# Kernel optimization log

Measured on AMD Instinct MI355X. Metric: run time of the kernel, lower is better.

Reference implementation:

```python
import jax, jax.numpy as jnp
import numpy as np

D_MODEL = 1024
N_HEADS = 16
D_LATENT = 64
LN_EPS = 1e-5


def setup_inputs() -> dict:
    key = jax.random.key(0)
    ks = jax.random.split(key, 9)
    dm, h, dl = D_MODEL, N_HEADS, D_LATENT
    hd = h * dl
    # xavier_uniform with gain=0.1: limit = 0.1 * sqrt(6/(fan_in+fan_out))
    def xavier(k, fan_in, fan_out):
        lim = 0.1 * np.sqrt(6.0 / (fan_in + fan_out))
        return jax.random.uniform(k, (fan_in, fan_out), jnp.float32, -lim, lim)
    return {
        "x": jax.random.normal(ks[0], (4, 2048, dm), jnp.float32),
        "ln_g": jnp.ones((dm,), jnp.float32),
        "ln_b": jnp.zeros((dm,), jnp.float32),
        "wq": xavier(ks[1], dm, hd), "bq": jnp.zeros((hd,), jnp.float32),
        "wk": xavier(ks[2], dm, hd), "bk": jnp.zeros((hd,), jnp.float32),
        "wv": xavier(ks[3], dm, hd), "bv": jnp.zeros((hd,), jnp.float32),
        "wo": xavier(ks[4], hd, dm), "bo": jnp.zeros((dm,), jnp.float32),
    }


def reference(x, ln_g, ln_b, wq, bq, wk, bk, wv, bv, wo, bo):
    b, s, dm = x.shape
    h, dl = N_HEADS, D_LATENT
    # context = raw x (bound before LayerNorm in the torch code)
    context = x
    mu = jnp.mean(x, axis=-1, keepdims=True)
    var = jnp.var(x, axis=-1, keepdims=True)
    xn = (x - mu) * jax.lax.rsqrt(var + LN_EPS) * ln_g + ln_b
    q = (xn @ wq + bq).reshape(b, s, h, dl).transpose(0, 2, 1, 3)          # b h s d
    k = (context @ wk + bk).reshape(b, -1, h, dl).transpose(0, 2, 1, 3)    # b h t d
    v = (context @ wv + bv).reshape(b, -1, h, dl).transpose(0, 2, 1, 3)
    scores = jnp.einsum("bhsd,bhtd->bhst", q, k) / jnp.sqrt(jnp.float32(dl))
    attn = jax.nn.softmax(scores.astype(jnp.float32), axis=-1)
    # dropout omitted (eval mode / deterministic reference)
    out = jnp.einsum("bhst,bhtd->bhsd", attn, v)
    out = out.transpose(0, 2, 1, 3).reshape(b, s, h * dl)
    return out @ wo + bo
```

## Files before the change

### kernel.cpp

```cpp
#include <hip/hip_runtime.h>
#include <cstdint>

typedef __attribute__((ext_vector_type(8))) __bf16 bf16x8;
typedef __attribute__((ext_vector_type(8))) unsigned short u16x8;
typedef __attribute__((ext_vector_type(4))) unsigned short u16x4;
typedef __attribute__((ext_vector_type(4))) float f32x4;
typedef __attribute__((ext_vector_type(2))) unsigned int u32x2;
typedef __attribute__((ext_vector_type(4))) unsigned int u32x4;

__device__ inline unsigned short f2bf(float f) {
  return __builtin_bit_cast(unsigned short, (__bf16)f);
}

__device__ inline void llds16(const void* g, void* l) {
  __builtin_amdgcn_global_load_lds((const uint32_t*)g, (uint32_t*)l, 16, 0, 0);
}

__device__ inline bf16x8 ldfrag(const unsigned short* p) {
  u16x8 v = *(const u16x8*)p;
  return __builtin_bit_cast(bf16x8, v);
}

__device__ inline f32x4 mfma16(bf16x8 a, bf16x8 b, f32x4 c) {
  return __builtin_amdgcn_mfma_f32_16x16x32_bf16(a, b, c, 0, 0, 0);
}

__global__ __launch_bounds__(256) void ln_kernel(
    const float* __restrict__ x, const float* __restrict__ g, const float* __restrict__ be,
    unsigned short* __restrict__ xn, unsigned short* __restrict__ xb)
{
  const int row = blockIdx.x, tid = threadIdx.x;
  const size_t base = (size_t)row * 1024 + tid * 4;
  float4 v = *(const float4*)&x[base];
  float s  = v.x + v.y + v.z + v.w;
  float sq = v.x*v.x + v.y*v.y + v.z*v.z + v.w*v.w;
#pragma unroll
  for (int o = 1; o < 64; o <<= 1) { s += __shfl_xor(s, o); sq += __shfl_xor(sq, o); }
  __shared__ float ls[8];
  if ((tid & 63) == 0) { ls[tid >> 6] = s; ls[4 + (tid >> 6)] = sq; }
  __syncthreads();
  s  = ls[0] + ls[1] + ls[2] + ls[3];
  sq = ls[4] + ls[5] + ls[6] + ls[7];
  const float mu   = s * (1.f / 1024.f);
  const float var  = sq * (1.f / 1024.f) - mu * mu;
  const float rstd = rsqrtf(var + 1e-5f);
  float4 gv = *(const float4*)&g[tid * 4];
  float4 bv = *(const float4*)&be[tid * 4];
  u16x4 a, bb;
  a[0] = f2bf((v.x - mu) * rstd * gv.x + bv.x);
  a[1] = f2bf((v.y - mu) * rstd * gv.y + bv.y);
  a[2] = f2bf((v.z - mu) * rstd * gv.z + bv.z);
  a[3] = f2bf((v.w - mu) * rstd * gv.w + bv.w);
  bb[0] = f2bf(v.x); bb[1] = f2bf(v.y); bb[2] = f2bf(v.z); bb[3] = f2bf(v.w);
  *(u16x4*)&xn[base] = a;
  *(u16x4*)&xb[base] = bb;
}

__global__ __launch_bounds__(256) void wcast_kernel(
    const float* __restrict__ wq, const float* __restrict__ wk,
    const float* __restrict__ wv, const float* __restrict__ wo,
    unsigned short* __restrict__ wT, unsigned short* __restrict__ woT)
{
  __shared__ float t[64][66];
  const int z = blockIdx.z;
  const float* W = (z == 0) ? wq : (z == 1) ? wk : (z == 2) ? wv : wo;
  unsigned short* O = (z < 3) ? (wT + (size_t)z * 1048576) : woT;
  const int n0 = blockIdx.x * 64, k0 = blockIdx.y * 64;
  for (int idx = threadIdx.x; idx < 4096; idx += 256) {
    int r = idx >> 6, c = idx & 63;
    t[r][c] = W[(size_t)(k0 + r) * 1024 + n0 + c];
  }
  __syncthreads();
  for (int idx = threadIdx.x; idx < 4096; idx += 256) {
    int r = idx >> 6, c = idx & 63;
    O[(size_t)(n0 + r) * 1024 + k0 + c] = f2bf(t[c][r]);
  }
}

__global__ __launch_bounds__(256) void vtrans_kernel(
    const unsigned short* __restrict__ V, unsigned short* __restrict__ VT)
{
  __shared__ unsigned short t[64][66];
  const int bh = blockIdx.y, t0 = blockIdx.x * 64;
  const unsigned short* src = V + (size_t)bh * 131072 + (size_t)t0 * 64;
  for (int idx = threadIdx.x; idx < 4096; idx += 256) {
    int r = idx >> 6, c = idx & 63;
    t[r][c] = src[(size_t)r * 64 + c];
  }
  __syncthreads();
  unsigned short* dst = VT + (size_t)bh * 131072 + t0;
  for (int idx = threadIdx.x; idx < 4096; idx += 256) {
    int r = idx >> 6, c = idx & 63;
    dst[(size_t)r * 2048 + c] = t[c][r];
  }
}

template<int MODE>
__global__ __launch_bounds__(256) void gemm_kernel(
    const unsigned short* __restrict__ A0, const unsigned short* __restrict__ A1,
    const unsigned short* __restrict__ BT,
    const float* __restrict__ b0, const float* __restrict__ b1, const float* __restrict__ b2,
    void* __restrict__ Cv, int M, int N, int K)
{
  __shared__ unsigned short S[32768];
  const int tid = threadIdx.x;
  const int wave = tid >> 6, lane = tid & 63;
  const int l15 = lane & 15, l4 = lane >> 4;
  const int swz = (l15 & 7) << 3;
  const int NBN = N >> 7;
  const int nwg = gridDim.x, cpx = nwg >> 3;
  const int orig = blockIdx.x;
  const int id = (orig & 7) * cpx + (orig >> 3);
  const int bn = id % NBN, bm = id / NBN;
  const int m0 = bm * 128, n0 = bn * 128;
  const unsigned short* Ap = (MODE == 0 && bn >= 8) ? A1 : A0;
  const int wr = (wave >> 1) * 64, wc = (wave & 1) * 64;

  f32x4 acc[4][4];
#pragma unroll
  for (int m = 0; m < 4; m++)
#pragma unroll
    for (int n = 0; n < 4; n++) acc[m][n] = {0.f, 0.f, 0.f, 0.f};

  auto STAGE = [&](int b, int kt) {
#pragma unroll
    for (int r = 0; r < 4; r++) {
      int D = r * 4096 + tid * 16;
      int row = D >> 7;
      int colus = ((D & 127) >> 1) ^ ((row & 7) << 3);
      llds16(&Ap[(size_t)(m0 + row) * K + kt + colus], &S[b * 16384 + r * 2048 + wave * 512]);
      llds16(&BT[(size_t)(n0 + row) * K + kt + colus],
             &S[b * 16384 + 8192 + r * 2048 + wave * 512]);
    }
  };

  const int KSTEPS = K >> 6;
  int cur = 0;
  STAGE(0, 0);
  for (int ki = 0; ki < KSTEPS; ki++) {
    if (ki < KSTEPS - 1) {
      STAGE(cur ^ 1, (ki + 1) << 6);
      asm volatile("s_waitcnt vmcnt(8)" ::: "memory");
    } else {
      asm volatile("s_waitcnt vmcnt(0)" ::: "memory");
    }
    __builtin_amdgcn_s_barrier();
    __builtin_amdgcn_sched_barrier(0);
    const unsigned short* Asb = &S[cur * 16384];
    const unsigned short* Bsb = &S[cur * 16384 + 8192];
#pragma unroll
    for (int ks = 0; ks < 2; ks++) {
      bf16x8 af[4], bfr[4];
#pragma unroll
      for (int m = 0; m < 4; m++)
        af[m]  = ldfrag(&Asb[(wr + m * 16 + l15) * 64 + ((ks * 32 + l4 * 8) ^ swz)]);
#pragma unroll
      for (int n = 0; n < 4; n++)
        bfr[n] = ldfrag(&Bsb[(wc + n * 16 + l15) * 64 + ((ks * 32 + l4 * 8) ^ swz)]);
#pragma unroll
      for (int m = 0; m < 4; m++)
#pragma unroll
        for (int n = 0; n < 4; n++)
          acc[m][n] = mfma16(af[m], bfr[n], acc[m][n]);
    }
    __builtin_amdgcn_s_barrier();
    cur ^= 1;
  }

#pragma unroll
  for (int nf = 0; nf < 4; nf++) {
    int c = n0 + wc + nf * 16 + l15;
    float bias; float sc = 1.0f;
    if (MODE == 0) {
      int sec = c >> 10;
      bias = (sec == 0 ? b0 : (sec == 1 ? b1 : b2))[c & 1023];
      if (sec == 0) sc = 0.18033688011112042f;
    } else {
      bias = b0[c];
    }
#pragma unroll
    for (int mf = 0; mf < 4; mf++) {
#pragma unroll
      for (int reg = 0; reg < 4; reg++) {
        int rrow = m0 + wr + mf * 16 + l4 * 4 + reg;
        float v = acc[mf][nf][reg] + bias;
        if (MODE == 0) {
          int sec = c >> 10, h = (c >> 6) & 15, d = c & 63;
          int b = rrow >> 11, t = rrow & 2047;
          ((unsigned short*)Cv)[(size_t)sec * 8388608 +
                                ((size_t)(b * 16 + h) * 2048 + t) * 64 + d] = f2bf(v * sc);
        } else {
          ((float*)Cv)[(size_t)rrow * N + c] = v;
        }
      }
    }
  }
}

__global__ __launch_bounds__(512, 4) void attn_kernel(
    const unsigned short* __restrict__ Q,
    const unsigned short* __restrict__ Kg,
    const unsigned short* __restrict__ VTg,
    unsigned short* __restrict__ Oa)
{
  __shared__ unsigned short S[32768];
  const int tid = threadIdx.x;
  const int wave = tid >> 6, lane = tid & 63;
  const int l15 = lane & 15, l4 = lane >> 4;
  const int swz = (l15 & 7) << 3;
  const int orig = blockIdx.x;
  const int wg = ((orig & 7) << 6) + (orig >> 3);
  const int qb = wg & 7, bh = wg >> 3;
  const size_t bhbase = (size_t)bh * 131072;
  const int q0 = qb * 256 + wave * 32;

  const u16x8 onesu = {0x3F80, 0x3F80, 0x3F80, 0x3F80, 0x3F80, 0x3F80, 0x3F80, 0x3F80};
  const bf16x8 ones = __builtin_bit_cast(bf16x8, onesu);

  bf16x8 qf[2][2];
#pragma unroll
  for (int m = 0; m < 2; m++)
#pragma unroll
    for (int ks = 0; ks < 2; ks++)
      qf[m][ks] = ldfrag(&Q[bhbase + (size_t)(q0 + m * 16 + l15) * 64 + ks * 32 + l4 * 8]);

  f32x4 accO[2][4];
#pragma unroll
  for (int m = 0; m < 2; m++)
#pragma unroll
    for (int n = 0; n < 4; n++) accO[m][n] = {0.f, 0.f, 0.f, 0.f};
  f32x4 accR[2] = {{0.f, 0.f, 0.f, 0.f}, {0.f, 0.f, 0.f, 0.f}};

  auto STAGE = [&](int b, int jj) {
#pragma unroll
    for (int r = 0; r < 2; r++) {
      int D = r * 8192 + tid * 16;
      int rowK = D >> 7;
      int colKus = ((D & 127) >> 1) ^ ((rowK & 7) << 3);
      llds16(&Kg[bhbase + (size_t)(jj * 128 + rowK) * 64 + colKus],
             &S[b * 16384 + r * 4096 + wave * 512]);
      int rowV = D >> 8;
      int colVus = ((D & 255) >> 1) ^ ((rowV & 7) << 3);
      llds16(&VTg[bhbase + (size_t)rowV * 2048 + jj * 128 + colVus],
             &S[b * 16384 + 8192 + r * 4096 + wave * 512]);
    }
  };

  int cur = 0;
  STAGE(0, 0);
  for (int j = 0; j < 16; j++) {
    if (j < 15) {
      STAGE(cur ^ 1, j + 1);
      asm volatile("s_waitcnt vmcnt(4)" ::: "memory");
    } else {
      asm volatile("s_waitcnt vmcnt(0)" ::: "memory");
    }
    __builtin_amdgcn_s_barrier();
    __builtin_amdgcn_sched_barrier(0);

    const unsigned short* Kb = &S[cur * 16384];
    const unsigned short* Vb = &S[cur * 16384 + 8192];

#pragma unroll
    for (int kt = 0; kt < 4; kt++) {
      bf16x8 kf00 = ldfrag(&Kb[((2 * kt) * 16 + l15) * 64 + ((0 * 32 + l4 * 8) ^ swz)]);
      bf16x8 kf01 = ldfrag(&Kb[((2 * kt) * 16 + l15) * 64 + ((1 * 32 + l4 * 8) ^ swz)]);
      bf16x8 kf10 = ldfrag(&Kb[((2 * kt + 1) * 16 + l15) * 64 + ((0 * 32 + l4 * 8) ^ swz)]);
      bf16x8 kf11 = ldfrag(&Kb[((2 * kt + 1) * 16 + l15) * 64 + ((1 * 32 + l4 * 8) ^ swz)]);
      f32x4 sa = {0.f, 0.f, 0.f, 0.f}, sb = sa, sc = sa, sd = sa;
      __builtin_amdgcn_s_setprio(1);
      sa = mfma16(kf00, qf[0][0], sa); sb = mfma16(kf00, qf[1][0], sb);
      sc = mfma16(kf10, qf[0][0], sc); sd = mfma16(kf10, qf[1][0], sd);
      sa = mfma16(kf01, qf[0][1], sa); sb = mfma16(kf01, qf[1][1], sb);
      sc = mfma16(kf11, qf[0][1], sc); sd = mfma16(kf11, qf[1][1], sd);
      __builtin_amdgcn_s_setprio(0);

      bf16x8 vf[4];
#pragma unroll
      for (int n = 0; n < 4; n++)
        vf[n] = ldfrag(&Vb[(n * 16 + l15) * 128 + ((kt * 32 + l4 * 8) ^ swz)]);

      bf16x8 pf[2];
#pragma unroll
      for (int m = 0; m < 2; m++) {
        const f32x4 se = (m == 0) ? sa : sb;
        const f32x4 so = (m == 0) ? sc : sd;
        uint32_t V0, V1, V2, V3;
        {
          u16x4 pk;
#pragma unroll
          for (int r = 0; r < 4; r++) pk[r] = f2bf(__builtin_amdgcn_exp2f(se[r]));
          u32x2 w = __builtin_bit_cast(u32x2, pk);
          V0 = w[0]; V1 = w[1];
        }
        {
          u16x4 pk;
#pragma unroll
          for (int r = 0; r < 4; r++) pk[r] = f2bf(__builtin_amdgcn_exp2f(so[r]));
          u32x2 w = __builtin_bit_cast(u32x2, pk);
          V2 = w[0]; V3 = w[1];
        }
        asm("s_nop 1\n\t"
            "v_permlane32_swap_b32 %0, %2\n\t"
            "v_permlane32_swap_b32 %1, %3\n\t"
            "v_permlane16_swap_b32 %0, %2\n\t"
            "v_permlane16_swap_b32 %1, %3"
            : "+v"(V0), "+v"(V1), "+v"(V2), "+v"(V3));
        u32x4 fw = {V0, V1, V2, V3};
        pf[m] = __builtin_bit_cast(bf16x8, fw);
      }

      __builtin_amdgcn_s_setprio(1);
#pragma unroll
      for (int m = 0; m < 2; m++) {
        accR[m] = mfma16(pf[m], ones, accR[m]);
#pragma unroll
        for (int n = 0; n < 4; n++)
          accO[m][n] = mfma16(pf[m], vf[n], accO[m][n]);
      }
      __builtin_amdgcn_s_setprio(0);
    }

    __builtin_amdgcn_s_barrier();
    cur ^= 1;
  }

  const int b = bh >> 4, h = bh & 15;
#pragma unroll
  for (int m = 0; m < 2; m++)
#pragma unroll
    for (int reg = 0; reg < 4; reg++) {
      float inv = 1.0f / accR[m][reg];
      int srow = q0 + m * 16 + l4 * 4 + reg;
#pragma unroll
      for (int n = 0; n < 4; n++) {
        float v = accO[m][n][reg] * inv;
        Oa[((size_t)(b * 2048) + srow) * 1024 + h * 64 + n * 16 + l15] = f2bf(v);
      }
    }
}

extern "C" void kernel_launch(void* const* d_in, const int* in_sizes, int n_in,
                              void* d_out, int out_size, void* d_ws, size_t ws_size,
                              hipStream_t stream) {
  (void)in_sizes; (void)n_in; (void)out_size; (void)ws_size;
  const float* x   = (const float*)d_in[0];
  const float* lng = (const float*)d_in[1];
  const float* lnb = (const float*)d_in[2];
  const float* wq  = (const float*)d_in[3];
  const float* bq  = (const float*)d_in[4];
  const float* wk  = (const float*)d_in[5];
  const float* bk  = (const float*)d_in[6];
  const float* wv  = (const float*)d_in[7];
  const float* bv  = (const float*)d_in[8];
  const float* wo  = (const float*)d_in[9];
  const float* bo  = (const float*)d_in[10];

  unsigned short* ws = (unsigned short*)d_ws;
  const size_t NE = 8388608;
  unsigned short* xn  = ws;
  unsigned short* xb  = ws + NE;
  unsigned short* wT  = ws + 2 * NE;
  unsigned short* woT = wT + 3145728;
  unsigned short* qkv = woT + 1048576;
  unsigned short* vT  = xn;
  unsigned short* oat = xb;

  wcast_kernel<<<dim3(16, 16, 4), 256, 0, stream>>>(wq, wk, wv, wo, wT, woT);
  ln_kernel<<<dim3(8192), 256, 0, stream>>>(x, lng, lnb, xn, xb);
  gemm_kernel<0><<<dim3(1536), 256, 0, stream>>>(xn, xb, wT, bq, bk, bv, qkv, 8192, 3072, 1024);
  vtrans_kernel<<<dim3(32, 64), 256, 0, stream>>>(qkv + 2 * NE, vT);
  attn_kernel<<<dim3(512), 512, 0, stream>>>(qkv, qkv + NE, vT, oat);
  gemm_kernel<1><<<dim3(512), 256, 0, stream>>>(oat, oat, woT, bo, bo, bo, d_out, 8192, 1024, 1024);
}
```

Before: 182.9 us.

## Give each attention wave 64 query rows with 256-thread blocks

The attention kernel now runs with 4 waves per block instead of 8, and each wave handles 64 query rows instead of 32. Each K/V fragment read from LDS is therefore reused across twice as many MFMAs, which cuts LDS read traffic per unit of work. The K/V staging loop is rebalanced to 4 passes per thread, with the wait count adjusted to match. In exchange, each wave needs roughly twice the accumulator and score registers, and the block has fewer waves to hide latency, which can lower occupancy.

Result: no change. 185.4 us (+1.4%).

```diff
diff --git a/kernel.cpp b/kernel.cpp
--- a/kernel.cpp
+++ b/kernel.cpp
@@ -197,7 +197,7 @@
   }
 }
 
-__global__ __launch_bounds__(512, 4) void attn_kernel(
+__global__ __launch_bounds__(256, 2) void attn_kernel(
     const unsigned short* __restrict__ Q,
     const unsigned short* __restrict__ Kg,
     const unsigned short* __restrict__ VTg,
@@ -212,37 +212,39 @@
   const int wg = ((orig & 7) << 6) + (orig >> 3);
   const int qb = wg & 7, bh = wg >> 3;
   const size_t bhbase = (size_t)bh * 131072;
-  const int q0 = qb * 256 + wave * 32;
+  const int q0 = qb * 256 + wave * 64;
 
   const u16x8 onesu = {0x3F80, 0x3F80, 0x3F80, 0x3F80, 0x3F80, 0x3F80, 0x3F80, 0x3F80};
   const bf16x8 ones = __builtin_bit_cast(bf16x8, onesu);
 
-  bf16x8 qf[2][2];
-#pragma unroll
-  for (int m = 0; m < 2; m++)
+  bf16x8 qf[4][2];
+#pragma unroll
+  for (int m = 0; m < 4; m++)
 #pragma unroll
     for (int ks = 0; ks < 2; ks++)
       qf[m][ks] = ldfrag(&Q[bhbase + (size_t)(q0 + m * 16 + l15) * 64 + ks * 32 + l4 * 8]);
 
-  f32x4 accO[2][4];
-#pragma unroll
-  for (int m = 0; m < 2; m++)
+  f32x4 accO[4][4];
+#pragma unroll
+  for (int m = 0; m < 4; m++)
 #pragma unroll
     for (int n = 0; n < 4; n++) accO[m][n] = {0.f, 0.f, 0.f, 0.f};
-  f32x4 accR[2] = {{0.f, 0.f, 0.f, 0.f}, {0.f, 0.f, 0.f, 0.f}};
+  f32x4 accR[4];
+#pragma unroll
+  for (int m = 0; m < 4; m++) accR[m] = {0.f, 0.f, 0.f, 0.f};
 
   auto STAGE = [&](int b, int jj) {
 #pragma unroll
-    for (int r = 0; r < 2; r++) {
-      int D = r * 8192 + tid * 16;
+    for (int r = 0; r < 4; r++) {
+      int D = r * 4096 + tid * 16;
       int rowK = D >> 7;
       int colKus = ((D & 127) >> 1) ^ ((rowK & 7) << 3);
       llds16(&Kg[bhbase + (size_t)(jj * 128 + rowK) * 64 + colKus],
-             &S[b * 16384 + r * 4096 + wave * 512]);
+             &S[b * 16384 + r * 2048 + wave * 512]);
       int rowV = D >> 8;
       int colVus = ((D & 255) >> 1) ^ ((rowV & 7) << 3);
       llds16(&VTg[bhbase + (size_t)rowV * 2048 + jj * 128 + colVus],
-             &S[b * 16384 + 8192 + r * 4096 + wave * 512]);
+             &S[b * 16384 + 8192 + r * 2048 + wave * 512]);
     }
   };
 
@@ -251,7 +253,7 @@
   for (int j = 0; j < 16; j++) {
     if (j < 15) {
       STAGE(cur ^ 1, j + 1);
-      asm volatile("s_waitcnt vmcnt(4)" ::: "memory");
+      asm volatile("s_waitcnt vmcnt(8)" ::: "memory");
     } else {
       asm volatile("s_waitcnt vmcnt(0)" ::: "memory");
     }
@@ -263,16 +265,27 @@
 
 #pragma unroll
     for (int kt = 0; kt < 4; kt++) {
-      bf16x8 kf00 = ldfrag(&Kb[((2 * kt) * 16 + l15) * 64 + ((0 * 32 + l4 * 8) ^ swz)]);
-      bf16x8 kf01 = ldfrag(&Kb[((2 * kt) * 16 + l15) * 64 + ((1 * 32 + l4 * 8) ^ swz)]);
-      bf16x8 kf10 = ldfrag(&Kb[((2 * kt + 1) * 16 + l15) * 64 + ((0 * 32 + l4 * 8) ^ swz)]);
-      bf16x8 kf11 = ldfrag(&Kb[((2 * kt + 1) * 16 + l15) * 64 + ((1 * 32 + l4 * 8) ^ swz)]);
-      f32x4 sa = {0.f, 0.f, 0.f, 0.f}, sb = sa, sc = sa, sd = sa;
+      bf16x8 kf[2][2];
+#pragma unroll
+      for (int tf2 = 0; tf2 < 2; tf2++)
+#pragma unroll
+        for (int ks = 0; ks < 2; ks++)
+          kf[tf2][ks] =
+              ldfrag(&Kb[((2 * kt + tf2) * 16 + l15) * 64 + ((ks * 32 + l4 * 8) ^ swz)]);
+
+      f32x4 st[2][4];
+#pragma unroll
+      for (int tf2 = 0; tf2 < 2; tf2++)
+#pragma unroll
+        for (int m = 0; m < 4; m++) st[tf2][m] = {0.f, 0.f, 0.f, 0.f};
       __builtin_amdgcn_s_setprio(1);
-      sa = mfma16(kf00, qf[0][0], sa); sb = mfma16(kf00, qf[1][0], sb);
-      sc = mfma16(kf10, qf[0][0], sc); sd = mfma16(kf10, qf[1][0], sd);
-      sa = mfma16(kf01, qf[0][1], sa); sb = mfma16(kf01, qf[1][1], sb);
-      sc = mfma16(kf11, qf[0][1], sc); sd = mfma16(kf11, qf[1][1], sd);
+#pragma unroll
+      for (int ks = 0; ks < 2; ks++)
+#pragma unroll
+        for (int tf2 = 0; tf2 < 2; tf2++)
+#pragma unroll
+          for (int m = 0; m < 4; m++)
+            st[tf2][m] = mfma16(kf[tf2][ks], qf[m][ks], st[tf2][m]);
       __builtin_amdgcn_s_setprio(0);
 
       bf16x8 vf[4];
@@ -280,23 +293,21 @@
       for (int n = 0; n < 4; n++)
         vf[n] = ldfrag(&Vb[(n * 16 + l15) * 128 + ((kt * 32 + l4 * 8) ^ swz)]);
 
-      bf16x8 pf[2];
-#pragma unroll
-      for (int m = 0; m < 2; m++) {
-        const f32x4 se = (m == 0) ? sa : sb;
-        const f32x4 so = (m == 0) ? sc : sd;
+      bf16x8 pf[4];
+#pragma unroll
+      for (int m = 0; m < 4; m++) {
         uint32_t V0, V1, V2, V3;
         {
           u16x4 pk;
 #pragma unroll
-          for (int r = 0; r < 4; r++) pk[r] = f2bf(__builtin_amdgcn_exp2f(se[r]));
+          for (int r = 0; r < 4; r++) pk[r] = f2bf(__builtin_amdgcn_exp2f(st[0][m][r]));
           u32x2 w = __builtin_bit_cast(u32x2, pk);
           V0 = w[0]; V1 = w[1];
         }
         {
           u16x4 pk;
 #pragma unroll
-          for (int r = 0; r < 4; r++) pk[r] = f2bf(__builtin_amdgcn_exp2f(so[r]));
+          for (int r = 0; r < 4; r++) pk[r] = f2bf(__builtin_amdgcn_exp2f(st[1][m][r]));
           u32x2 w = __builtin_bit_cast(u32x2, pk);
           V2 = w[0]; V3 = w[1];
         }
@@ -312,7 +323,7 @@
 
       __builtin_amdgcn_s_setprio(1);
 #pragma unroll
-      for (int m = 0; m < 2; m++) {
+      for (int m = 0; m < 4; m++) {
         accR[m] = mfma16(pf[m], ones, accR[m]);
 #pragma unroll
         for (int n = 0; n < 4; n++)
@@ -327,7 +338,7 @@
 
   const int b = bh >> 4, h = bh & 15;
 #pragma unroll
-  for (int m = 0; m < 2; m++)
+  for (int m = 0; m < 4; m++)
 #pragma unroll
     for (int reg = 0; reg < 4; reg++) {
       float inv = 1.0f / accR[m][reg];
@@ -370,6 +381,6 @@
   ln_kernel<<<dim3(8192), 256, 0, stream>>>(x, lng, lnb, xn, xb);
   gemm_kernel<0><<<dim3(1536), 256, 0, stream>>>(xn, xb, wT, bq, bk, bv, qkv, 8192, 3072, 1024);
   vtrans_kernel<<<dim3(32, 64), 256, 0, stream>>>(qkv + 2 * NE, vT);
-  attn_kernel<<<dim3(512), 512, 0, stream>>>(qkv, qkv + NE, vT, oat);
+  attn_kernel<<<dim3(512), 256, 0, stream>>>(qkv, qkv + NE, vT, oat);
   gemm_kernel<1><<<dim3(512), 256, 0, stream>>>(oat, oat, woT, bo, bo, bo, d_out, 8192, 1024, 1024);
 }
```
